# Kernel tuning notes

Hardware: AMD Instinct MI355X
Metric: run time of the kernel (lower is better)

## Reference

```python
import jax, jax.numpy as jnp
import numpy as np

HEADS = 8
DIM_HEAD = 64
WINDOW = 256
CAUSAL = True


def _sliding_window_mask(seq_len: int, window: int, causal: bool) -> jnp.ndarray:
    i = jnp.arange(seq_len)[:, None]
    j = jnp.arange(seq_len)[None, :]
    # attend iff i - window + 1 <= j <= i + window - 1 (end_pos exclusive)
    mask = (j >= i - window + 1) & (j <= i + window - 1)
    if causal:
        mask = mask & (j <= i)
    return mask  # (S, S) bool


def setup_inputs() -> dict:
    key = jax.random.key(0)
    k1, k2, k3 = jax.random.split(key, 3)
    dim = 512
    inner = HEADS * DIM_HEAD
    x = jax.random.normal(k1, (2, 2048, dim), dtype=jnp.float32)
    W_qkv = jax.random.normal(k2, (dim, 3 * inner), dtype=jnp.float32) * 0.02
    W_out = jax.random.normal(k3, (inner, dim), dtype=jnp.float32) * 0.02
    return {"x": x, "W_qkv": W_qkv, "W_out": W_out}


def reference(x, W_qkv, W_out):
    B, S, D = x.shape
    H, Dh = HEADS, DIM_HEAD
    scale = Dh ** (-0.5)
    qkv = x @ W_qkv  # (B, S, 3*H*Dh)
    q, k, v = jnp.split(qkv, 3, axis=-1)
    q = q.reshape(B, S, H, Dh).transpose(0, 2, 1, 3)  # (B, H, S, Dh)
    k = k.reshape(B, S, H, Dh).transpose(0, 2, 1, 3)
    v = v.reshape(B, S, H, Dh).transpose(0, 2, 1, 3)
    scores = jnp.einsum('bhid,bhjd->bhij', q, k) * scale
    mask = _sliding_window_mask(S, WINDOW, CAUSAL)
    mask_value = -jnp.finfo(scores.dtype).max
    scores = jnp.where(mask[None, None, :, :], scores, mask_value)
    attn = jax.nn.softmax(scores, axis=-1)  # (B, H, S, S)
    out = jnp.einsum('bhij,bhjd->bhid', attn, v)
    out = out.transpose(0, 2, 1, 3).reshape(B, S, H * Dh)
    out = out @ W_out  # (B, S, D)
    return (out, attn)
```

## Files before the change

### kernel.cpp

```cpp
#include <hip/hip_runtime.h>
#include <hip/hip_bf16.h>

typedef __bf16 bf16x8 __attribute__((ext_vector_type(8)));
typedef float f32x4 __attribute__((ext_vector_type(4)));

#define MFMA16(a,b,c) __builtin_amdgcn_mfma_f32_16x16x32_bf16(a, b, c, 0, 0, 0)

typedef const __attribute__((address_space(1))) void* gas_t;
typedef __attribute__((address_space(3))) void* las_t;

__device__ inline void gload16(const __bf16* g, __bf16* lds) {
  __builtin_amdgcn_global_load_lds((gas_t)g, (las_t)lds, 16, 0, 0);
}

__device__ inline void fill_attn_rows(float* __restrict__ attn, int rowStart, int rowEnd,
                                      int tid) {
  const f32x4 z4 = {0.f, 0.f, 0.f, 0.f};
  for (int g = rowStart; g < rowEnd; g++) {
    const int bh = g >> 11, i = g & 2047;
    const int qt = i >> 6;
    const int lo = qt >= 4 ? (qt - 4) << 6 : 0;
    const int hi = (qt + 1) << 6;
    float* rp = attn + ((size_t)bh << 22) + ((size_t)i << 11);
    for (int j = tid << 2; j < lo; j += 1024)
      __builtin_nontemporal_store(z4, reinterpret_cast<f32x4*>(rp + j));
    for (int j = hi + (tid << 2); j < 2048; j += 1024)
      __builtin_nontemporal_store(z4, reinterpret_cast<f32x4*>(rp + j));
  }
}

__device__ inline void fill_block_chunk(float* __restrict__ attn, int fillStart, int fillEnd,
                                        int fid, int nfill, int tid) {
  const int total = fillEnd - fillStart;
  const int per = (total + nfill - 1) / nfill;
  const int myStart = fillStart + fid * per;
  int myEnd = myStart + per;
  if (myEnd > fillEnd) myEnd = fillEnd;
  if (myStart < myEnd) fill_attn_rows(attn, myStart, myEnd, tid);
}

__device__ inline void transpose_body(const float* __restrict__ in, __bf16* __restrict__ out,
                                      int R, int C, int tile, int tid, float (*t)[65]) {
  const int tilesC = C >> 6;
  const int tc = tile % tilesC, tr = tile / tilesC;
  const int r0 = tr << 6, c0 = tc << 6;
  const int ri = tid >> 2, cq = (tid & 3) << 4;
#pragma unroll
  for (int e = 0; e < 16; e += 4) {
    float4 v = *reinterpret_cast<const float4*>(&in[(size_t)(r0 + ri) * C + c0 + cq + e]);
    t[ri][cq + e]     = v.x;
    t[ri][cq + e + 1] = v.y;
    t[ri][cq + e + 2] = v.z;
    t[ri][cq + e + 3] = v.w;
  }
  __syncthreads();
  const int co = tid >> 2, rq = (tid & 3) << 4;
  __attribute__((aligned(16))) __bf16 buf[16];
#pragma unroll
  for (int e = 0; e < 16; e++) buf[e] = (__bf16)t[rq + e][co];
  *reinterpret_cast<bf16x8*>(&out[(size_t)(c0 + co) * R + r0 + rq])     = *reinterpret_cast<bf16x8*>(&buf[0]);
  *reinterpret_cast<bf16x8*>(&out[(size_t)(c0 + co) * R + r0 + rq + 8]) = *reinterpret_cast<bf16x8*>(&buf[8]);
}

__global__ __launch_bounds__(256) void prep(const float* __restrict__ Wqkv,
                                            const float* __restrict__ Wout,
                                            __bf16* __restrict__ Wqt,
                                            __bf16* __restrict__ Wot) {
  __shared__ float t[64][65];
  const int bid = blockIdx.x, tid = threadIdx.x;
  if (bid < 192) transpose_body(Wqkv, Wqt, 512, 1536, bid, tid, t);
  else           transpose_body(Wout, Wot, 512, 512, bid - 192, tid, t);
}

template <typename AT, typename OT>
__global__ __launch_bounds__(256) void gemm_bt(const AT* __restrict__ A,
                                               const __bf16* __restrict__ Bt,
                                               OT* __restrict__ C, int M, int N, int K,
                                               float* __restrict__ fillAttn,
                                               int fillStart, int fillEnd, int gxCompute) {
  constexpr bool AF32 = (sizeof(AT) == 4);
  constexpr int ASZ = AF32 ? 128 * 72 * 2 : 128 * 64 * 2;
  __shared__ __align__(16) char asbuf[ASZ];
  __shared__ __align__(16) __bf16 BsL[128 * 64];
  const int tid = threadIdx.x;

  if ((int)blockIdx.x >= gxCompute) {
    const int nfx = gridDim.x - gxCompute;
    const int fid = (blockIdx.x - gxCompute) + nfx * blockIdx.y;
    fill_block_chunk(fillAttn, fillStart, fillEnd, fid, nfx * gridDim.y, tid);
    return;
  }

  const int wave = tid >> 6, lane = tid & 63;
  const int c = lane & 15, q4 = lane >> 4;
  const int bm = blockIdx.y << 7, bn = blockIdx.x << 7;
  const int wm = (wave >> 1) << 6, wn = (wave & 1) << 6;
  f32x4 acc[4][4];
#pragma unroll
  for (int m = 0; m < 4; m++)
#pragma unroll
    for (int n = 0; n < 4; n++)
#pragma unroll
      for (int e = 0; e < 4; e++) acc[m][n][e] = 0.f;

  __bf16 (*AsP)[72] = (AF32 ? (__bf16 (*)[72])asbuf : nullptr);
  __bf16* AsL = (__bf16*)asbuf;

  const int srow8 = lane >> 3;
  const int sseg  = lane & 7;
  auto stage_async = [&](const __bf16* src, __bf16* dst, int rowBase, int k0) {
#pragma unroll
    for (int i = 0; i < 4; i++) {
      const int rb = (wave << 5) + (i << 3);
      const int rr = rb + srow8;
      const int cs = sseg ^ (rr & 7);
      gload16(src + (size_t)(rowBase + rr) * K + k0 + cs * 8, dst + rb * 64);
    }
  };

  const int srow = tid >> 1, scol = (tid & 1) << 5;
  bf16x8 av[4];
  auto loadA_f32 = [&](int k0) {
    const AT* ag = A + (size_t)(bm + srow) * K + k0 + scol;
#pragma unroll
    for (int r = 0; r < 4; r++) {
      float4 lo = *reinterpret_cast<const float4*>(ag + r * 8);
      float4 hi = *reinterpret_cast<const float4*>(ag + r * 8 + 4);
      bf16x8 v;
      v[0] = (__bf16)lo.x; v[1] = (__bf16)lo.y; v[2] = (__bf16)lo.z; v[3] = (__bf16)lo.w;
      v[4] = (__bf16)hi.x; v[5] = (__bf16)hi.y; v[6] = (__bf16)hi.z; v[7] = (__bf16)hi.w;
      av[r] = v;
    }
  };

  if constexpr (AF32) loadA_f32(0);

  for (int k0 = 0; k0 < K; k0 += 64) {
    __syncthreads();
    if constexpr (AF32) {
#pragma unroll
      for (int r = 0; r < 4; r++)
        *reinterpret_cast<bf16x8*>(&AsP[srow][scol + r * 8]) = av[r];
    } else {
      stage_async((const __bf16*)A, AsL, bm, k0);
    }
    stage_async(Bt, BsL, bn, k0);
    __syncthreads();
    if constexpr (AF32) {
      if (k0 + 64 < K) loadA_f32(k0 + 64);
    }
#pragma unroll
    for (int ks = 0; ks < 2; ks++) {
      const int kk = ks * 32 + q4 * 8;
      bf16x8 af[4], bfv[4];
#pragma unroll
      for (int m = 0; m < 4; m++) {
        const int row = wm + m * 16 + c;
        if constexpr (AF32) af[m] = *reinterpret_cast<const bf16x8*>(&AsP[row][kk]);
        else af[m] = *reinterpret_cast<const bf16x8*>(&AsL[row * 64 + ((ks * 4 + q4) ^ (row & 7)) * 8]);
      }
#pragma unroll
      for (int n = 0; n < 4; n++) {
        const int row = wn + n * 16 + c;
        bfv[n] = *reinterpret_cast<const bf16x8*>(&BsL[row * 64 + ((ks * 4 + q4) ^ (row & 7)) * 8]);
      }
#pragma unroll
      for (int m = 0; m < 4; m++)
#pragma unroll
        for (int n = 0; n < 4; n++) acc[m][n] = MFMA16(af[m], bfv[n], acc[m][n]);
    }
  }
#pragma unroll
  for (int m = 0; m < 4; m++)
#pragma unroll
    for (int n = 0; n < 4; n++)
#pragma unroll
      for (int r2 = 0; r2 < 4; r2++) {
        const int row = bm + wm + m * 16 + q4 * 4 + r2;
        const int col = bn + wn + n * 16 + c;
        C[(size_t)row * N + col] = (OT)acc[m][n][r2];
      }
}

__global__ __launch_bounds__(256) void attn_fused(const __bf16* __restrict__ QKV,
                                                  float* __restrict__ attn,
                                                  __bf16* __restrict__ AO) {
  __shared__ __align__(16) __bf16 KV[2][64][72];
  __shared__ __align__(16) __bf16 Pw[4][16][72];
  const int tid = threadIdx.x;

  if (blockIdx.x >= 32) {
    const int fid = (blockIdx.x - 32) + (gridDim.x - 32) * blockIdx.y;
    fill_block_chunk(attn, 9000, 25000, fid, (gridDim.x - 32) * gridDim.y, tid);
    return;
  }

  const int qt = blockIdx.x, bh = blockIdx.y;
  const int b = bh >> 3, h = bh & 7;
  const int qi0 = qt << 6;
  const int wave = tid >> 6, lane = tid & 63;
  const int c = lane & 15, q4 = lane >> 4;
  const int base = b * 2048;
  const int r = tid >> 2, qq = (tid & 3) << 4;

  bf16x8 qf0, qf1;
  {
    const __bf16* s = QKV + (size_t)(base + qi0 + wave * 16 + c) * 1536 + h * 64 + q4 * 8;
    qf0 = *reinterpret_cast<const bf16x8*>(s);
    qf1 = *reinterpret_cast<const bf16x8*>(s + 32);
  }

  f32x4 acc[5][4];
#pragma unroll
  for (int t = 0; t < 5; t++)
#pragma unroll
    for (int ct = 0; ct < 4; ct++)
#pragma unroll
      for (int e = 0; e < 4; e++) acc[t][ct][e] = 0.f;

  const int tfirst = qt >= 4 ? 0 : 4 - qt;
  bf16x8 kv0, kv1;
  {
    const __bf16* s = QKV + (size_t)(base + ((qt - 4 + tfirst) << 6) + r) * 1536 + 512 + h * 64 + qq;
    kv0 = *reinterpret_cast<const bf16x8*>(s);
    kv1 = *reinterpret_cast<const bf16x8*>(s + 8);
  }
  int cur = 0;
#pragma unroll
  for (int t = 0; t < 5; t++) {
    if (qt - 4 + t < 0) continue;
    *reinterpret_cast<bf16x8*>(&KV[cur][r][qq]) = kv0;
    *reinterpret_cast<bf16x8*>(&KV[cur][r][qq + 8]) = kv1;
    if (t < 4) {
      const __bf16* s = QKV + (size_t)(base + ((qt - 3 + t) << 6) + r) * 1536 + 512 + h * 64 + qq;
      kv0 = *reinterpret_cast<const bf16x8*>(s);
      kv1 = *reinterpret_cast<const bf16x8*>(s + 8);
    }
    __syncthreads();
#pragma unroll
    for (int ks = 0; ks < 2; ks++) {
      const int kk = ks * 32 + q4 * 8;
      const bf16x8 af = ks ? qf1 : qf0;
#pragma unroll
      for (int ct = 0; ct < 4; ct++) {
        bf16x8 bfr = *reinterpret_cast<const bf16x8*>(&KV[cur][ct * 16 + c][kk]);
        acc[t][ct] = MFMA16(af, bfr, acc[t][ct]);
      }
    }
    cur ^= 1;
  }

  const float scale = 0.125f;
  const int igBase = qi0 + wave * 16 + q4 * 4;
#pragma unroll
  for (int t = 0; t < 5; t++) {
#pragma unroll
    for (int ct = 0; ct < 4; ct++) {
      const int jb = ((qt - 4 + t) << 6) + ct * 16 + c;
#pragma unroll
      for (int r2 = 0; r2 < 4; r2++) {
        const int ig = igBase + r2;
        const bool valid = (jb >= 0) && (jb <= ig) && (jb >= ig - 255);
        acc[t][ct][r2] = valid ? acc[t][ct][r2] * scale : -1e30f;
      }
    }
  }

  float pm[4];
#pragma unroll
  for (int r2 = 0; r2 < 4; r2++) {
    float v = acc[0][0][r2];
#pragma unroll
    for (int t = 0; t < 5; t++)
#pragma unroll
      for (int ct = 0; ct < 4; ct++) v = fmaxf(v, acc[t][ct][r2]);
    pm[r2] = v;
  }
#pragma unroll
  for (int off = 8; off >= 1; off >>= 1)
#pragma unroll
    for (int r2 = 0; r2 < 4; r2++) pm[r2] = fmaxf(pm[r2], __shfl_xor(pm[r2], off, 64));

  float ps[4] = {0.f, 0.f, 0.f, 0.f};
#pragma unroll
  for (int t = 0; t < 5; t++)
#pragma unroll
    for (int ct = 0; ct < 4; ct++)
#pragma unroll
      for (int r2 = 0; r2 < 4; r2++) {
        float p = __expf(acc[t][ct][r2] - pm[r2]);
        acc[t][ct][r2] = p;
        ps[r2] += p;
      }
#pragma unroll
  for (int off = 8; off >= 1; off >>= 1)
#pragma unroll
    for (int r2 = 0; r2 < 4; r2++) ps[r2] += __shfl_xor(ps[r2], off, 64);

#pragma unroll
  for (int r2 = 0; r2 < 4; r2++) ps[r2] = 1.0f / ps[r2];
#pragma unroll
  for (int t = 0; t < 5; t++)
#pragma unroll
    for (int ct = 0; ct < 4; ct++)
#pragma unroll
      for (int r2 = 0; r2 < 4; r2++) acc[t][ct][r2] *= ps[r2];

  __syncthreads();

  f32x4 o[4];
#pragma unroll
  for (int n = 0; n < 4; n++)
#pragma unroll
    for (int e = 0; e < 4; e++) o[n][e] = 0.f;

  const int jv = tid >> 2, dqa = tid & 3;
  bf16x8 vr0, vr1;
  {
    const __bf16* s = QKV + (size_t)(base + ((qt - 4 + tfirst) << 6) + jv) * 1536 + 1024 + h * 64;
    vr0 = *reinterpret_cast<const bf16x8*>(s + dqa * 8);
    vr1 = *reinterpret_cast<const bf16x8*>(s + (dqa + 4) * 8);
  }
  int pcur = 0;
#pragma unroll
  for (int t = 0; t < 5; t++) {
    if (qt - 4 + t < 0) continue;
#pragma unroll
    for (int ct = 0; ct < 4; ct++)
#pragma unroll
      for (int r2 = 0; r2 < 4; r2++)
        Pw[wave][q4 * 4 + r2][ct * 16 + c] = (__bf16)acc[t][ct][r2];
#pragma unroll
    for (int e = 0; e < 8; e++) {
      KV[pcur][dqa * 8 + e][jv] = vr0[e];
      KV[pcur][(dqa + 4) * 8 + e][jv] = vr1[e];
    }
    if (t < 4) {
      const __bf16* s = QKV + (size_t)(base + ((qt - 3 + t) << 6) + jv) * 1536 + 1024 + h * 64;
      vr0 = *reinterpret_cast<const bf16x8*>(s + dqa * 8);
      vr1 = *reinterpret_cast<const bf16x8*>(s + (dqa + 4) * 8);
    }
    __syncthreads();
#pragma unroll
    for (int ks = 0; ks < 2; ks++) {
      const int kk = ks * 32 + q4 * 8;
      bf16x8 af = *reinterpret_cast<const bf16x8*>(&Pw[wave][c][kk]);
#pragma unroll
      for (int n = 0; n < 4; n++) {
        bf16x8 bfr = *reinterpret_cast<const bf16x8*>(&KV[pcur][n * 16 + c][kk]);
        o[n] = MFMA16(af, bfr, o[n]);
      }
    }
    pcur ^= 1;
  }

  float* arow = attn + ((size_t)bh << 22);
#pragma unroll
  for (int r2 = 0; r2 < 4; r2++) {
    const int ig = igBase + r2;
    float* rowp = arow + ((size_t)ig << 11);
#pragma unroll
    for (int t = 0; t < 5; t++) {
      const int jt0 = (qt - 4 + t) << 6;
      if (jt0 < 0) continue;
#pragma unroll
      for (int ct = 0; ct < 4; ct++) {
        const int jb = jt0 + ct * 16 + c;
        rowp[jb] = acc[t][ct][r2];
      }
    }
  }

#pragma unroll
  for (int n = 0; n < 4; n++)
#pragma unroll
    for (int r2 = 0; r2 < 4; r2++)
      Pw[wave][q4 * 4 + r2][n * 16 + c] = (__bf16)o[n][r2];
  {
    const int er = lane >> 2;
    const int ec = (lane & 3) << 4;
    bf16x8 a0 = *reinterpret_cast<const bf16x8*>(&Pw[wave][er][ec]);
    bf16x8 a1 = *reinterpret_cast<const bf16x8*>(&Pw[wave][er][ec + 8]);
    __bf16* adst = AO + (size_t)(base + qi0 + wave * 16 + er) * 512 + h * 64 + ec;
    *reinterpret_cast<bf16x8*>(adst) = a0;
    *reinterpret_cast<bf16x8*>(adst + 8) = a1;
  }
}

extern "C" void kernel_launch(void* const* d_in, const int* in_sizes, int n_in,
                              void* d_out, int out_size, void* d_ws, size_t ws_size,
                              hipStream_t stream) {
  const float* x = (const float*)d_in[0];
  const float* Wqkv = (const float*)d_in[1];
  const float* Wout = (const float*)d_in[2];
  float* out = (float*)d_out;
  float* attn = out + (size_t)2 * 2048 * 512;

  char* ws = (char*)d_ws;
  __bf16* Wqt  = (__bf16*)(ws);
  __bf16* Wot  = (__bf16*)(ws + 1572864);
  __bf16* QKVb = (__bf16*)(ws + 1572864 + 524288);
  __bf16* AOb  = (__bf16*)(ws + 1572864 + 524288 + 12582912);

  prep<<<256, 256, 0, stream>>>(Wqkv, Wout, Wqt, Wot);

  gemm_bt<float, __bf16><<<dim3(24, 32), 256, 0, stream>>>(x, Wqt, QKVb, 4096, 1536, 512,
                                                           attn, 0, 9000, 12);

  attn_fused<<<dim3(48, 16), 256, 0, stream>>>(QKVb, attn, AOb);

  gemm_bt<__bf16, float><<<dim3(12, 32), 256, 0, stream>>>(AOb, Wot, out, 4096, 512, 512,
                                                           attn, 25000, 32768, 4);
}
```

Measured before the change: 84.81 us.

## Write full attention rows from attention kernel instead of spreading zero-fill

Removes the extra zero-fill blocks that were attached to the QKV GEMM, the attention kernel and the output GEMM. Each attention block now stages its 64x320 probability tile in shared memory as bf16 and writes complete 2048-wide rows (zeros outside the band) with coalesced nontemporal vector stores. The AO output is written directly from registers instead of through an LDS transpose. This trades overlap of the zero-fill with GEMM compute for fully coalesced row writes from one kernel. It also rounds the stored attention probabilities to bf16, which reduces their precision.

```diff
diff --git a/kernel.cpp b/kernel.cpp
--- a/kernel.cpp
+++ b/kernel.cpp
@@ -2,6 +2,7 @@
 #include <hip/hip_bf16.h>
 
 typedef __bf16 bf16x8 __attribute__((ext_vector_type(8)));
+typedef __bf16 bf16x4 __attribute__((ext_vector_type(4)));
 typedef float f32x4 __attribute__((ext_vector_type(4)));
 
 #define MFMA16(a,b,c) __builtin_amdgcn_mfma_f32_16x16x32_bf16(a, b, c, 0, 0, 0)
@@ -11,32 +12,6 @@
 
 __device__ inline void gload16(const __bf16* g, __bf16* lds) {
   __builtin_amdgcn_global_load_lds((gas_t)g, (las_t)lds, 16, 0, 0);
-}
-
-__device__ inline void fill_attn_rows(float* __restrict__ attn, int rowStart, int rowEnd,
-                                      int tid) {
-  const f32x4 z4 = {0.f, 0.f, 0.f, 0.f};
-  for (int g = rowStart; g < rowEnd; g++) {
-    const int bh = g >> 11, i = g & 2047;
-    const int qt = i >> 6;
-    const int lo = qt >= 4 ? (qt - 4) << 6 : 0;
-    const int hi = (qt + 1) << 6;
-    float* rp = attn + ((size_t)bh << 22) + ((size_t)i << 11);
-    for (int j = tid << 2; j < lo; j += 1024)
-      __builtin_nontemporal_store(z4, reinterpret_cast<f32x4*>(rp + j));
-    for (int j = hi + (tid << 2); j < 2048; j += 1024)
-      __builtin_nontemporal_store(z4, reinterpret_cast<f32x4*>(rp + j));
-  }
-}
-
-__device__ inline void fill_block_chunk(float* __restrict__ attn, int fillStart, int fillEnd,
-                                        int fid, int nfill, int tid) {
-  const int total = fillEnd - fillStart;
-  const int per = (total + nfill - 1) / nfill;
-  const int myStart = fillStart + fid * per;
-  int myEnd = myStart + per;
-  if (myEnd > fillEnd) myEnd = fillEnd;
-  if (myStart < myEnd) fill_attn_rows(attn, myStart, myEnd, tid);
 }
 
 __device__ inline void transpose_body(const float* __restrict__ in, __bf16* __restrict__ out,
@@ -75,21 +50,12 @@
 template <typename AT, typename OT>
 __global__ __launch_bounds__(256) void gemm_bt(const AT* __restrict__ A,
                                                const __bf16* __restrict__ Bt,
-                                               OT* __restrict__ C, int M, int N, int K,
-                                               float* __restrict__ fillAttn,
-                                               int fillStart, int fillEnd, int gxCompute) {
+                                               OT* __restrict__ C, int M, int N, int K) {
   constexpr bool AF32 = (sizeof(AT) == 4);
   constexpr int ASZ = AF32 ? 128 * 72 * 2 : 128 * 64 * 2;
   __shared__ __align__(16) char asbuf[ASZ];
   __shared__ __align__(16) __bf16 BsL[128 * 64];
   const int tid = threadIdx.x;
-
-  if ((int)blockIdx.x >= gxCompute) {
-    const int nfx = gridDim.x - gxCompute;
-    const int fid = (blockIdx.x - gxCompute) + nfx * blockIdx.y;
-    fill_block_chunk(fillAttn, fillStart, fillEnd, fid, nfx * gridDim.y, tid);
-    return;
-  }
 
   const int wave = tid >> 6, lane = tid & 63;
   const int c = lane & 15, q4 = lane >> 4;
@@ -185,15 +151,11 @@
 __global__ __launch_bounds__(256) void attn_fused(const __bf16* __restrict__ QKV,
                                                   float* __restrict__ attn,
                                                   __bf16* __restrict__ AO) {
-  __shared__ __align__(16) __bf16 KV[2][64][72];
-  __shared__ __align__(16) __bf16 Pw[4][16][72];
+  __shared__ __align__(16) char smem[64 * 328 * 2];
+  __bf16 (*KV)[64][72] = reinterpret_cast<__bf16 (*)[64][72]>(smem);
+  __bf16 (*Pw)[16][72] = reinterpret_cast<__bf16 (*)[16][72]>(smem + 18432);
+  __bf16 (*Ps)[328]    = reinterpret_cast<__bf16 (*)[328]>(smem);
   const int tid = threadIdx.x;
-
-  if (blockIdx.x >= 32) {
-    const int fid = (blockIdx.x - 32) + (gridDim.x - 32) * blockIdx.y;
-    fill_block_chunk(attn, 9000, 25000, fid, (gridDim.x - 32) * gridDim.y, tid);
-    return;
-  }
 
   const int qt = blockIdx.x, bh = blockIdx.y;
   const int b = bh >> 3, h = bh & 7;
@@ -354,36 +316,39 @@
     pcur ^= 1;
   }
 
-  float* arow = attn + ((size_t)bh << 22);
-#pragma unroll
-  for (int r2 = 0; r2 < 4; r2++) {
-    const int ig = igBase + r2;
-    float* rowp = arow + ((size_t)ig << 11);
-#pragma unroll
-    for (int t = 0; t < 5; t++) {
-      const int jt0 = (qt - 4 + t) << 6;
-      if (jt0 < 0) continue;
-#pragma unroll
-      for (int ct = 0; ct < 4; ct++) {
-        const int jb = jt0 + ct * 16 + c;
-        rowp[jb] = acc[t][ct][r2];
-      }
-    }
-  }
-
 #pragma unroll
   for (int n = 0; n < 4; n++)
 #pragma unroll
-    for (int r2 = 0; r2 < 4; r2++)
-      Pw[wave][q4 * 4 + r2][n * 16 + c] = (__bf16)o[n][r2];
-  {
-    const int er = lane >> 2;
-    const int ec = (lane & 3) << 4;
-    bf16x8 a0 = *reinterpret_cast<const bf16x8*>(&Pw[wave][er][ec]);
-    bf16x8 a1 = *reinterpret_cast<const bf16x8*>(&Pw[wave][er][ec + 8]);
-    __bf16* adst = AO + (size_t)(base + qi0 + wave * 16 + er) * 512 + h * 64 + ec;
-    *reinterpret_cast<bf16x8*>(adst) = a0;
-    *reinterpret_cast<bf16x8*>(adst + 8) = a1;
+    for (int r2 = 0; r2 < 4; r2++) {
+      const int i = igBase + r2;
+      const int d = n * 16 + c;
+      AO[(size_t)(base + i) * 512 + h * 64 + d] = (__bf16)o[n][r2];
+    }
+
+  __syncthreads();
+#pragma unroll
+  for (int t = 0; t < 5; t++) {
+    if (qt - 4 + t < 0) continue;
+#pragma unroll
+    for (int ct = 0; ct < 4; ct++)
+#pragma unroll
+      for (int r2 = 0; r2 < 4; r2++)
+        Ps[wave * 16 + q4 * 4 + r2][t * 64 + ct * 16 + c] = (__bf16)acc[t][ct][r2];
+  }
+  __syncthreads();
+
+  const int ofs = (qt - 4) << 6;
+  float* tilebase = attn + ((size_t)bh << 22) + ((size_t)qi0 << 11);
+  for (int g = tid; g < 64 * 512; g += 256) {
+    const int row = g >> 9;
+    const int j0 = (g & 511) << 2;
+    const int local = j0 - ofs;
+    f32x4 w = {0.f, 0.f, 0.f, 0.f};
+    if ((unsigned)local < 320u) {
+      bf16x4 p = *reinterpret_cast<const bf16x4*>(&Ps[row][local]);
+      w[0] = (float)p[0]; w[1] = (float)p[1]; w[2] = (float)p[2]; w[3] = (float)p[3];
+    }
+    __builtin_nontemporal_store(w, reinterpret_cast<f32x4*>(tilebase + ((size_t)row << 11) + j0));
   }
 }
 
@@ -404,11 +369,9 @@
 
   prep<<<256, 256, 0, stream>>>(Wqkv, Wout, Wqt, Wot);
 
-  gemm_bt<float, __bf16><<<dim3(24, 32), 256, 0, stream>>>(x, Wqt, QKVb, 4096, 1536, 512,
-                                                           attn, 0, 9000, 12);
-
-  attn_fused<<<dim3(48, 16), 256, 0, stream>>>(QKVb, attn, AOb);
-
-  gemm_bt<__bf16, float><<<dim3(12, 32), 256, 0, stream>>>(AOb, Wot, out, 4096, 512, 512,
-                                                           attn, 25000, 32768, 4);
-}
+  gemm_bt<float, __bf16><<<dim3(12, 32), 256, 0, stream>>>(x, Wqt, QKVb, 4096, 1536, 512);
+
+  attn_fused<<<dim3(32, 16), 256, 0, stream>>>(QKVb, attn, AOb);
+
+  gemm_bt<__bf16, float><<<dim3(4, 32), 256, 0, stream>>>(AOb, Wot, out, 4096, 512, 512);
+}
```

After: 111.1 us. +31.0%, slower.
